# Performance work log

Hardware: AMD Instinct MI355X
Metric: run time of the kernel (lower is better)

## Reference

```python
import jax, jax.numpy as jnp
import numpy as np

B, IN, S, PD, P, D = 8192, 19000, 256, 128, 16, 64  # batch, input_dim, shared_dim, pathway_dim, n_pathways, n_drugs


def setup_inputs() -> dict:
    key = jax.random.key(0)
    ks = jax.random.split(key, 6)
    x = jax.random.normal(ks[0], (B, IN), dtype=jnp.float32)
    drug_indices = jax.random.randint(ks[1], (B,), 0, D, dtype=jnp.int32)
    W1 = jax.random.normal(ks[2], (IN, S), dtype=jnp.float32) / np.float32(np.sqrt(IN))
    b1 = jnp.zeros((S,), jnp.float32)
    Wp = jax.random.normal(ks[3], (P, S, PD), dtype=jnp.float32) / np.float32(np.sqrt(S))
    bp = jnp.zeros((P, PD), jnp.float32)
    Wd = jax.random.normal(ks[4], (D, PD), dtype=jnp.float32) / np.float32(np.sqrt(PD))
    bd = jnp.zeros((D,), jnp.float32)
    drug_to_pw = (jnp.arange(D, dtype=jnp.int32) % P)  # drug -> pathway routing table (i%16 per init_kwargs)
    return dict(x=x, drug_indices=drug_indices, W1=W1, b1=b1, Wp=Wp, bp=bp, Wd=Wd, bd=bd, drug_to_pw=drug_to_pw)


def reference(x, drug_indices, W1, b1, Wp, bp, Wd, bd, drug_to_pw):
    # shared encoder (dropout is identity in eval)
    h = jax.nn.relu(x @ W1 + b1)                                  # [B, S]
    # run all pathway experts densely (P is small), then per-sample select
    all_pw = jax.nn.relu(jnp.einsum('bs,psd->bpd', h, Wp) + bp)   # [B, P, PD]
    pw_idx = drug_to_pw[drug_indices]                             # [B]
    pw_out = jnp.take_along_axis(all_pw, pw_idx[:, None, None], axis=1)[:, 0]  # [B, PD]
    # per-sample drug head: gather row of Wd and dot
    out = jnp.sum(pw_out * Wd[drug_indices], axis=-1) + bd[drug_indices]       # [B]
    return out
```

## Files before the change

### kernel.cpp

```cpp
#include <hip/hip_runtime.h>

#define KREAL 19000
#define KP    19008
#define NSTEPS 594
#define BM 128
#define BN 256
#define MBLK 64
#define BATCH 8192
#define SDIM 256
#define PDIM 128
#define NPW  16
#define S2S  32
#define MAXBLK 272

typedef __attribute__((ext_vector_type(8))) short frag_ab;
typedef __attribute__((ext_vector_type(4))) float frag_cd;

static __device__ __forceinline__ short f2bf(float f) {
    union { float f; unsigned u; } cv; cv.f = f;
    unsigned u = cv.u;
    u += 0x7fffu + ((u >> 16) & 1u);
    return (short)(u >> 16);
}

static __device__ __forceinline__ short4 cvt4(float4 v) {
    short4 p;
    p.x = f2bf(v.x); p.y = f2bf(v.y); p.z = f2bf(v.z); p.w = f2bf(v.w);
    return p;
}

__global__ void transpose_w1(const float* __restrict__ W1, short* __restrict__ W1t) {
    __shared__ float tile[32][33];
    int k0 = blockIdx.x * 32;
    int n0 = blockIdx.y * 32;
    int tx = threadIdx.x & 31;
    int ty = threadIdx.x >> 5;
#pragma unroll
    for (int i = 0; i < 32; i += 8) {
        int k = k0 + ty + i;
        tile[ty + i][tx] = (k < KREAL) ? W1[(long)k * SDIM + n0 + tx] : 0.f;
    }
    __syncthreads();
#pragma unroll
    for (int i = 0; i < 32; i += 8) {
        int n = n0 + ty + i;
        W1t[(long)n * KP + k0 + tx] = f2bf(tile[tx][ty + i]);
    }
}

__global__ __launch_bounds__(1024)
void bucket(const int* __restrict__ drug_idx, const int* __restrict__ d2p,
            int* __restrict__ ord, int* __restrict__ blk_p) {
    __shared__ int cnt[NPW];
    __shared__ int pos[NPW];
    __shared__ int pstart[NPW];
    int t = threadIdx.x;
    if (t < NPW) { cnt[t] = 0; pos[t] = 0; }
    __syncthreads();

    int myp[8];
#pragma unroll
    for (int r = 0; r < 8; r++) {
        int i = t + r * 1024;
        myp[r] = d2p[drug_idx[i]];
        atomicAdd(&cnt[myp[r]], 1);
    }
    for (int i = t; i < MAXBLK * S2S; i += 1024) ord[i] = -1;
    if (t < MAXBLK) blk_p[t] = -1;
    __syncthreads();

    if (t == 0) {
        int bb = 0;
        for (int p = 0; p < NPW; p++) {
            pstart[p] = bb;
            bb += (cnt[p] + S2S - 1) / S2S;
        }
    }
    __syncthreads();

    if (t < NPW) {
        int p = t, nb = (cnt[p] + S2S - 1) / S2S, b0 = pstart[p];
        for (int j = 0; j < nb; j++) blk_p[b0 + j] = p;
    }
#pragma unroll
    for (int r = 0; r < 8; r++) {
        int i = t + r * 1024;
        int p = myp[r];
        int j = atomicAdd(&pos[p], 1);
        ord[pstart[p] * S2S + j] = i;
    }
}

__global__ __launch_bounds__(512, 2)
void gemm1(const float* __restrict__ x, const short* __restrict__ W1t,
           float* __restrict__ pout, int nch) {
    __shared__ short As[2][BM * 32];
    __shared__ short Bs[2][BN * 32];

    int bid = blockIdx.x;
    int mb, ch;
    if (nch == 4) {
        int xcd  = bid & 7;
        int slot = bid >> 3;
        ch = xcd >> 1;
        mb = ((xcd & 1) << 5) | slot;
    } else {
        mb = bid % MBLK;
        ch = bid / MBLK;
    }
    int m0 = mb * BM;
    int s0 = (NSTEPS * ch) / nch;
    int s1 = (NSTEPS * (ch + 1)) / nch;

    int tid  = threadIdx.x;
    int wave = tid >> 6;
    int lane = tid & 63;
    int wr = wave >> 2, wc = wave & 3;
    int lrow = lane & 15;
    int lq   = lane >> 4;

    int k4 = (tid & 7) << 2;
    const float* xp0 = x + (long)(m0 + (tid >> 3)) * KREAL + k4;
    const float* xp1 = xp0 + (long)64 * KREAL;
    const short* bp0 = W1t + (long)(tid >> 2) * KP + ((tid & 3) << 3);
    const short* bp1 = bp0 + (long)128 * KP;

    frag_cd acc[4][4];
#pragma unroll
    for (int i = 0; i < 4; i++)
#pragma unroll
        for (int j = 0; j < 4; j++) acc[i][j] = (frag_cd)(0.f);

    float4 ra0, ra1;
    int4   rb0, rb1;
    {
        int kb = s0 * 32;
        bool ok = (kb + k4 + 4 <= KREAL);
        ra0 = ok ? *(const float4*)(xp0 + kb) : make_float4(0.f, 0.f, 0.f, 0.f);
        ra1 = ok ? *(const float4*)(xp1 + kb) : make_float4(0.f, 0.f, 0.f, 0.f);
        rb0 = *(const int4*)(bp0 + kb);
        rb1 = *(const int4*)(bp1 + kb);
    }

    int buf = 0;
    for (int s = s0; s < s1; ++s) {
        *(short4*)(&As[buf][tid * 4])        = cvt4(ra0);
        *(short4*)(&As[buf][tid * 4 + 2048]) = cvt4(ra1);
        *(int4*)(&Bs[buf][tid * 8])          = rb0;
        *(int4*)(&Bs[buf][tid * 8 + 4096])   = rb1;
        if (s + 1 < s1) {
            int kb = (s + 1) * 32;
            bool ok = (kb + k4 + 4 <= KREAL);
            ra0 = ok ? *(const float4*)(xp0 + kb) : make_float4(0.f, 0.f, 0.f, 0.f);
            ra1 = ok ? *(const float4*)(xp1 + kb) : make_float4(0.f, 0.f, 0.f, 0.f);
            rb0 = *(const int4*)(bp0 + kb);
            rb1 = *(const int4*)(bp1 + kb);
        }
        __syncthreads();
        frag_ab af[4], bfr[4];
#pragma unroll
        for (int mt = 0; mt < 4; mt++)
            af[mt] = *(const frag_ab*)(&As[buf][(wr * 64 + mt * 16 + lrow) * 32 + lq * 8]);
#pragma unroll
        for (int nt = 0; nt < 4; nt++)
            bfr[nt] = *(const frag_ab*)(&Bs[buf][(wc * 64 + nt * 16 + lrow) * 32 + lq * 8]);
#pragma unroll
        for (int mt = 0; mt < 4; mt++)
#pragma unroll
            for (int nt = 0; nt < 4; nt++)
                acc[mt][nt] = __builtin_amdgcn_mfma_f32_16x16x32_bf16(
                    af[mt], bfr[nt], acc[mt][nt], 0, 0, 0);
        buf ^= 1;
    }

#pragma unroll
    for (int mt = 0; mt < 4; mt++)
#pragma unroll
        for (int nt = 0; nt < 4; nt++)
#pragma unroll
            for (int r = 0; r < 4; r++) {
                int row = m0 + wr * 64 + mt * 16 + lq * 4 + r;
                int col = wc * 64 + nt * 16 + lrow;
                pout[((long)ch * BATCH + row) * SDIM + col] = acc[mt][nt][r];
            }
}

__global__ __launch_bounds__(256)
void stage2(const float* __restrict__ pout, const float* __restrict__ b1,
            const float* __restrict__ Wp, const float* __restrict__ bp,
            const float* __restrict__ Wd, const float* __restrict__ bd,
            const int* __restrict__ drug_idx,
            const int* __restrict__ ord, const int* __restrict__ blk_p,
            float* __restrict__ out, int nch) {
    int g = blockIdx.x;
    int p = blk_p[g];
    if (p < 0) return;

    __shared__ float hs[S2S][260];
    __shared__ float pw[S2S][132];
    __shared__ int   sidx[S2S];

    int t = threadIdx.x;
    if (t < S2S) sidx[t] = ord[g * S2S + t];
    __syncthreads();

    int si = t >> 3, l8 = t & 7;
    int b = sidx[si];

#pragma unroll
    for (int v = 0; v < 8; v++) {
        int i = (l8 + v * 8) * 4;
        float4 a = *(const float4*)(b1 + i);
        if (b >= 0) {
            for (int c = 0; c < nch; c++) {
                float4 q = *(const float4*)(pout + ((long)c * BATCH + b) * SDIM + i);
                a.x += q.x; a.y += q.y; a.z += q.z; a.w += q.w;
            }
        }
        float4 r;
        r.x = fmaxf(a.x, 0.f); r.y = fmaxf(a.y, 0.f);
        r.z = fmaxf(a.z, 0.f); r.w = fmaxf(a.w, 0.f);
        *(float4*)(&hs[si][i]) = r;
    }
    __syncthreads();

    int d = t & 127, half = t >> 7;
    const float* wpc = Wp + (long)p * SDIM * PDIM + d;
    float acc[16];
#pragma unroll
    for (int jj = 0; jj < 16; jj++) acc[jj] = 0.f;
    for (int s4 = 0; s4 < SDIM; s4 += 4) {
        float w0 = wpc[(s4 + 0) * PDIM];
        float w1 = wpc[(s4 + 1) * PDIM];
        float w2 = wpc[(s4 + 2) * PDIM];
        float w3 = wpc[(s4 + 3) * PDIM];
#pragma unroll
        for (int jj = 0; jj < 16; jj++) {
            float4 h4 = *(const float4*)(&hs[half * 16 + jj][s4]);
            acc[jj] = fmaf(h4.x, w0, acc[jj]);
            acc[jj] = fmaf(h4.y, w1, acc[jj]);
            acc[jj] = fmaf(h4.z, w2, acc[jj]);
            acc[jj] = fmaf(h4.w, w3, acc[jj]);
        }
    }
    float bpv = bp[p * PDIM + d];
#pragma unroll
    for (int jj = 0; jj < 16; jj++)
        pw[half * 16 + jj][d] = fmaxf(acc[jj] + bpv, 0.f);
    __syncthreads();

    if (b >= 0) {
        int drug = drug_idx[b];
        const float* wd = Wd + drug * PDIM;
        float v = 0.f;
#pragma unroll
        for (int k = 0; k < 16; k++) {
            int dd = l8 + k * 8;
            v = fmaf(pw[si][dd], wd[dd], v);
        }
        v += __shfl_down(v, 4, 8);
        v += __shfl_down(v, 2, 8);
        v += __shfl_down(v, 1, 8);
        if (l8 == 0) out[b] = v + bd[drug];
    }
}

extern "C" void kernel_launch(void* const* d_in, const int* in_sizes, int n_in,
                              void* d_out, int out_size, void* d_ws, size_t ws_size,
                              hipStream_t stream) {
    const float* x    = (const float*)d_in[0];
    const int*   drug = (const int*)d_in[1];
    const float* W1   = (const float*)d_in[2];
    const float* b1   = (const float*)d_in[3];
    const float* Wp   = (const float*)d_in[4];
    const float* bp   = (const float*)d_in[5];
    const float* Wd   = (const float*)d_in[6];
    const float* bd   = (const float*)d_in[7];
    const int*   d2p  = (const int*)d_in[8];
    float* out = (float*)d_out;

    size_t pchunk    = (size_t)BATCH * SDIM * sizeof(float);
    size_t w1t_bytes = (size_t)SDIM * KP * sizeof(short);
    size_t ordb      = (size_t)MAXBLK * S2S * sizeof(int);
    size_t blkb      = (size_t)MAXBLK * sizeof(int);
    int nch = 4;
    if (ws_size < w1t_bytes + 4 * pchunk + ordb + blkb + 256) {
        long avail = (long)ws_size - (long)(w1t_bytes + ordb + blkb + 256);
        nch = (int)(avail / (long)pchunk);
        if (nch < 1) nch = 1;
        if (nch > 4) nch = 4;
    }
    float* pout  = (float*)d_ws;
    short* W1t   = (short*)((char*)d_ws + (size_t)nch * pchunk);
    int*   ord   = (int*)((char*)d_ws + (size_t)nch * pchunk + w1t_bytes);
    int*   blk_p = ord + MAXBLK * S2S;

    hipLaunchKernelGGL(transpose_w1, dim3(NSTEPS, SDIM / 32), dim3(256), 0, stream,
                       W1, W1t);
    hipLaunchKernelGGL(bucket, dim3(1), dim3(1024), 0, stream,
                       drug, d2p, ord, blk_p);
    hipLaunchKernelGGL(gemm1, dim3(MBLK * nch), dim3(512), 0, stream,
                       x, W1t, pout, nch);
    hipLaunchKernelGGL(stage2, dim3(MAXBLK), dim3(256), 0, stream,
                       pout, b1, Wp, bp, Wd, bd, drug, ord, blk_p, out, nch);
}
```

Before: 918.0 us.

## Fold bucketing into gemm1 as extra blocks and re-tile stage2 pathway matmul

```diff
diff --git a/kernel.cpp b/kernel.cpp
--- a/kernel.cpp
+++ b/kernel.cpp
@@ -29,12 +29,21 @@
     return p;
 }
 
-__global__ void transpose_w1(const float* __restrict__ W1, short* __restrict__ W1t) {
+__global__ void transpose_w1(const float* __restrict__ W1, short* __restrict__ W1t,
+                             int* __restrict__ ord, int* __restrict__ blk_p,
+                             int* __restrict__ gpos) {
     __shared__ float tile[32][33];
     int k0 = blockIdx.x * 32;
     int n0 = blockIdx.y * 32;
     int tx = threadIdx.x & 31;
     int ty = threadIdx.x >> 5;
+
+    if (blockIdx.x == 0 && blockIdx.y == 0) {
+        for (int i = threadIdx.x; i < MAXBLK * S2S; i += 256) ord[i] = -1;
+        for (int i = threadIdx.x; i < MAXBLK; i += 256) blk_p[i] = -1;
+        if (threadIdx.x < NPW) gpos[threadIdx.x] = 0;
+    }
+
 #pragma unroll
     for (int i = 0; i < 32; i += 8) {
         int k = k0 + ty + i;
@@ -48,56 +57,67 @@
     }
 }
 
-__global__ __launch_bounds__(1024)
-void bucket(const int* __restrict__ drug_idx, const int* __restrict__ d2p,
-            int* __restrict__ ord, int* __restrict__ blk_p) {
-    __shared__ int cnt[NPW];
-    __shared__ int pos[NPW];
-    __shared__ int pstart[NPW];
-    int t = threadIdx.x;
-    if (t < NPW) { cnt[t] = 0; pos[t] = 0; }
-    __syncthreads();
-
-    int myp[8];
-#pragma unroll
-    for (int r = 0; r < 8; r++) {
-        int i = t + r * 1024;
-        myp[r] = d2p[drug_idx[i]];
-        atomicAdd(&cnt[myp[r]], 1);
-    }
-    for (int i = t; i < MAXBLK * S2S; i += 1024) ord[i] = -1;
-    if (t < MAXBLK) blk_p[t] = -1;
-    __syncthreads();
-
-    if (t == 0) {
-        int bb = 0;
-        for (int p = 0; p < NPW; p++) {
-            pstart[p] = bb;
-            bb += (cnt[p] + S2S - 1) / S2S;
-        }
-    }
-    __syncthreads();
-
-    if (t < NPW) {
-        int p = t, nb = (cnt[p] + S2S - 1) / S2S, b0 = pstart[p];
-        for (int j = 0; j < nb; j++) blk_p[b0 + j] = p;
-    }
-#pragma unroll
-    for (int r = 0; r < 8; r++) {
-        int i = t + r * 1024;
-        int p = myp[r];
-        int j = atomicAdd(&pos[p], 1);
-        ord[pstart[p] * S2S + j] = i;
-    }
-}
-
 __global__ __launch_bounds__(512, 2)
 void gemm1(const float* __restrict__ x, const short* __restrict__ W1t,
-           float* __restrict__ pout, int nch) {
+           float* __restrict__ pout,
+           const int* __restrict__ drug_idx, const int* __restrict__ d2p,
+           int* __restrict__ ord, int* __restrict__ blk_p, int* __restrict__ gpos,
+           int nch) {
     __shared__ short As[2][BM * 32];
     __shared__ short Bs[2][BN * 32];
 
-    int bid = blockIdx.x;
+    int bid  = blockIdx.x;
+    int nblk = MBLK * nch;
+    int tid  = threadIdx.x;
+
+    if (bid >= nblk) {
+        int p = bid - nblk;
+        __shared__ int hist[8][NPW];
+        __shared__ int cnt[NPW];
+        int w = tid >> 6, lane = tid & 63;
+        if (tid < 8 * NPW) ((int*)hist)[tid] = 0;
+        __syncthreads();
+
+        int q[16];
+#pragma unroll
+        for (int r = 0; r < 16; r++)
+            q[r] = d2p[drug_idx[tid + 512 * r]];
+
+#pragma unroll 1
+        for (int r = 0; r < 16; r++) {
+#pragma unroll
+            for (int pw = 0; pw < NPW; pw++) {
+                unsigned long long m = __ballot(q[r] == pw);
+                if (lane == 0) hist[w][pw] += __popcll(m);
+            }
+        }
+        __syncthreads();
+        if (tid < NPW) {
+            int c = 0;
+            for (int w2 = 0; w2 < 8; w2++) c += hist[w2][tid];
+            cnt[tid] = c;
+        }
+        __syncthreads();
+
+        int pstart = 0;
+        for (int qq = 0; qq < p; qq++) pstart += (cnt[qq] + 31) >> 5;
+        int nb = (cnt[p] + 31) >> 5;
+        if (tid < nb) blk_p[pstart + tid] = p;
+
+        int base0 = pstart * S2S;
+#pragma unroll 1
+        for (int r = 0; r < 16; r++) {
+            unsigned long long m = __ballot(q[r] == p);
+            int rank = __popcll(m & ((1ull << lane) - 1ull));
+            int wcnt = __popcll(m);
+            int wbase = 0;
+            if (lane == 0 && wcnt) wbase = atomicAdd(gpos + p, wcnt);
+            wbase = __shfl(wbase, 0, 64);
+            if (q[r] == p) ord[base0 + wbase + rank] = tid + 512 * r;
+        }
+        return;
+    }
+
     int mb, ch;
     if (nch == 4) {
         int xcd  = bid & 7;
@@ -112,7 +132,6 @@
     int s0 = (NSTEPS * ch) / nch;
     int s1 = (NSTEPS * (ch + 1)) / nch;
 
-    int tid  = threadIdx.x;
     int wave = tid >> 6;
     int lane = tid & 63;
     int wr = wave >> 2, wc = wave & 3;
@@ -224,29 +243,37 @@
     }
     __syncthreads();
 
-    int d = t & 127, half = t >> 7;
+    int d   = t & 63;
+    int grp = t >> 6;
     const float* wpc = Wp + (long)p * SDIM * PDIM + d;
-    float acc[16];
-#pragma unroll
-    for (int jj = 0; jj < 16; jj++) acc[jj] = 0.f;
+    float acc0[8], acc1[8];
+#pragma unroll
+    for (int jj = 0; jj < 8; jj++) { acc0[jj] = 0.f; acc1[jj] = 0.f; }
+#pragma unroll 2
     for (int s4 = 0; s4 < SDIM; s4 += 4) {
-        float w0 = wpc[(s4 + 0) * PDIM];
-        float w1 = wpc[(s4 + 1) * PDIM];
-        float w2 = wpc[(s4 + 2) * PDIM];
-        float w3 = wpc[(s4 + 3) * PDIM];
-#pragma unroll
-        for (int jj = 0; jj < 16; jj++) {
-            float4 h4 = *(const float4*)(&hs[half * 16 + jj][s4]);
-            acc[jj] = fmaf(h4.x, w0, acc[jj]);
-            acc[jj] = fmaf(h4.y, w1, acc[jj]);
-            acc[jj] = fmaf(h4.z, w2, acc[jj]);
-            acc[jj] = fmaf(h4.w, w3, acc[jj]);
-        }
-    }
-    float bpv = bp[p * PDIM + d];
-#pragma unroll
-    for (int jj = 0; jj < 16; jj++)
-        pw[half * 16 + jj][d] = fmaxf(acc[jj] + bpv, 0.f);
+        float w00 = wpc[(s4 + 0) * PDIM], w01 = wpc[(s4 + 0) * PDIM + 64];
+        float w10 = wpc[(s4 + 1) * PDIM], w11 = wpc[(s4 + 1) * PDIM + 64];
+        float w20 = wpc[(s4 + 2) * PDIM], w21 = wpc[(s4 + 2) * PDIM + 64];
+        float w30 = wpc[(s4 + 3) * PDIM], w31 = wpc[(s4 + 3) * PDIM + 64];
+#pragma unroll
+        for (int jj = 0; jj < 8; jj++) {
+            float4 h4 = *(const float4*)(&hs[grp * 8 + jj][s4]);
+            acc0[jj] = fmaf(h4.x, w00, acc0[jj]);
+            acc1[jj] = fmaf(h4.x, w01, acc1[jj]);
+            acc0[jj] = fmaf(h4.y, w10, acc0[jj]);
+            acc1[jj] = fmaf(h4.y, w11, acc1[jj]);
+            acc0[jj] = fmaf(h4.z, w20, acc0[jj]);
+            acc1[jj] = fmaf(h4.z, w21, acc1[jj]);
+            acc0[jj] = fmaf(h4.w, w30, acc0[jj]);
+            acc1[jj] = fmaf(h4.w, w31, acc1[jj]);
+        }
+    }
+    float bpv0 = bp[p * PDIM + d], bpv1 = bp[p * PDIM + d + 64];
+#pragma unroll
+    for (int jj = 0; jj < 8; jj++) {
+        pw[grp * 8 + jj][d]      = fmaxf(acc0[jj] + bpv0, 0.f);
+        pw[grp * 8 + jj][d + 64] = fmaxf(acc1[jj] + bpv1, 0.f);
+    }
     __syncthreads();
 
     if (b >= 0) {
@@ -283,9 +310,10 @@
     size_t w1t_bytes = (size_t)SDIM * KP * sizeof(short);
     size_t ordb      = (size_t)MAXBLK * S2S * sizeof(int);
     size_t blkb      = (size_t)MAXBLK * sizeof(int);
+    size_t gposb     = (size_t)NPW * sizeof(int);
     int nch = 4;
-    if (ws_size < w1t_bytes + 4 * pchunk + ordb + blkb + 256) {
-        long avail = (long)ws_size - (long)(w1t_bytes + ordb + blkb + 256);
+    if (ws_size < w1t_bytes + 4 * pchunk + ordb + blkb + gposb + 256) {
+        long avail = (long)ws_size - (long)(w1t_bytes + ordb + blkb + gposb + 256);
         nch = (int)(avail / (long)pchunk);
         if (nch < 1) nch = 1;
         if (nch > 4) nch = 4;
@@ -294,13 +322,12 @@
     short* W1t   = (short*)((char*)d_ws + (size_t)nch * pchunk);
     int*   ord   = (int*)((char*)d_ws + (size_t)nch * pchunk + w1t_bytes);
     int*   blk_p = ord + MAXBLK * S2S;
+    int*   gpos  = blk_p + MAXBLK;
 
     hipLaunchKernelGGL(transpose_w1, dim3(NSTEPS, SDIM / 32), dim3(256), 0, stream,
-                       W1, W1t);
-    hipLaunchKernelGGL(bucket, dim3(1), dim3(1024), 0, stream,
-                       drug, d2p, ord, blk_p);
-    hipLaunchKernelGGL(gemm1, dim3(MBLK * nch), dim3(512), 0, stream,
-                       x, W1t, pout, nch);
+                       W1, W1t, ord, blk_p, gpos);
+    hipLaunchKernelGGL(gemm1, dim3(MBLK * nch + NPW), dim3(512), 0, stream,
+                       x, W1t, pout, drug, d2p, ord, blk_p, gpos, nch);
     hipLaunchKernelGGL(stage2, dim3(MAXBLK), dim3(256), 0, stream,
                        pout, b1, Wp, bp, Wd, bd, drug, ord, blk_p, out, nch);
 }
```

After: 896.7 us. 2.3% less time.
